# Kernel optimization log

Hardware: AMD Instinct MI355X
Metric: run time of the kernel (lower is better)

Reference implementation:

```python
import jax, jax.numpy as jnp
import numpy as np

N, D, H, DF = 2048, 1024, 16, 4096
DK = D // H
EPS = 1e-5


def layernorm(x, g, b):
    mu = jnp.mean(x, axis=-1, keepdims=True)
    var = jnp.mean((x - mu) ** 2, axis=-1, keepdims=True)
    return (x - mu) * jax.lax.rsqrt(var + EPS) * g + b


def setup_inputs() -> dict:
    key = jax.random.key(0)
    ks = jax.random.split(key, 8)
    s = 0.02
    return {
        "X": jax.random.normal(ks[0], (N, D), dtype=jnp.float32),
        "Wqkv": jax.random.normal(ks[1], (2 * D, D), dtype=jnp.float32) * s,
        "W1": jax.random.normal(ks[2], (DF, D), dtype=jnp.float32) * s,
        "b1": jnp.zeros((DF,), dtype=jnp.float32),
        "W2": jax.random.normal(ks[3], (D, DF), dtype=jnp.float32) * s,
        "b2": jnp.zeros((D,), dtype=jnp.float32),
        "g1": jnp.ones((D,), dtype=jnp.float32),
        "be1": jnp.zeros((D,), dtype=jnp.float32),
        "g2": jnp.ones((D,), dtype=jnp.float32),
        "be2": jnp.zeros((D,), dtype=jnp.float32),
    }


def reference(X, Wqkv, W1, b1, W2, b2, g1, be1, g2, be2):
    # shared-QK multi-head attention (Q == K), no bias
    qkv = X @ Wqkv.T                      # [N, 2D]
    qk, v = jnp.split(qkv, 2, axis=-1)    # [N, D] each
    qk = qk.reshape(N, H, DK)
    v = v.reshape(N, H, DK)
    scale = DK ** 0.5
    scores = jnp.einsum('nhd,mhd->hnm', qk, qk) / scale  # [H, N, N]
    att = jax.nn.softmax(scores, axis=-1)
    attn_out = jnp.einsum('hnm,mhd->nhd', att, v).reshape(N, D)
    # residual + LN, FFN (dropout is identity in eval), residual + LN
    h = layernorm(X + attn_out, g1, be1)
    ffn = jax.nn.relu(h @ W1.T + b1) @ W2.T + b2
    return layernorm(h + ffn, g2, be2)
```

## Files before the change

kernel.cpp:

```cpp
#include <hip/hip_runtime.h>
#include <stdint.h>


#define NTOK 2048
#define DMODEL 1024
#define NHEAD 16
#define DHEAD 64
#define DFF 4096

typedef __attribute__((ext_vector_type(8))) short short8;
typedef __attribute__((ext_vector_type(4))) short short4v;
typedef __attribute__((ext_vector_type(4))) float f32x4;

__device__ __forceinline__ float fexp2(float x) { return __builtin_amdgcn_exp2f(x); }

__device__ __forceinline__ short f2b(float f) {
  union { float f; unsigned u; } v; v.f = f;
  unsigned r = v.u + 0x7fffu + ((v.u >> 16) & 1u);
  return (short)(r >> 16);
}

__device__ __forceinline__ void gload_lds16(const void* g, void* l) {
  __builtin_amdgcn_global_load_lds((const __attribute__((address_space(1))) void*)g,
                                   (__attribute__((address_space(3))) void*)l,
                                   16, 0, 0);
}

__global__ void cast_all(const float* __restrict__ s0, short* __restrict__ d0, int n0,
                         const float* __restrict__ s1, short* __restrict__ d1, int n1,
                         const float* __restrict__ s2, short* __restrict__ d2, int n2,
                         const float* __restrict__ s3, short* __restrict__ d3, int n3) {
  int i = blockIdx.x * blockDim.x + threadIdx.x;
  const float* s; short* d; int j = i;
  if (j < n0) { s = s0; d = d0; }
  else { j -= n0;
    if (j < n1) { s = s1; d = d1; }
    else { j -= n1;
      if (j < n2) { s = s2; d = d2; }
      else { j -= n2; if (j >= n3) return; s = s3; d = d3; }
    }
  }
  const float4* p = (const float4*)(s + (size_t)j * 8);
  float4 a = p[0], b = p[1];
  short8 o;
  o[0] = f2b(a.x); o[1] = f2b(a.y); o[2] = f2b(a.z); o[3] = f2b(a.w);
  o[4] = f2b(b.x); o[5] = f2b(b.y); o[6] = f2b(b.z); o[7] = f2b(b.w);
  *(short8*)(d + (size_t)j * 8) = o;
}

template<int BM, int BN, int WR, int WC, bool BF16OUT, bool BIAS, bool RELU>
__launch_bounds__(WR * WC * 64, 2)
__global__ void gemm_bt(const short* __restrict__ A, const short* __restrict__ B,
                        const float* __restrict__ bias,
                        float* __restrict__ Cf, short* __restrict__ Cb,
                        int M, int N, int K, int lda, int ldb, int kstep) {
  constexpr int BK = 64;
  constexpr int THREADS = WR * WC * 64;
  constexpr int ACH = (BM * (BK / 8)) / THREADS;
  constexpr int BCH = (BN * (BK / 8)) / THREADS;
  constexpr int LPS = ACH + BCH;
  constexpr int MR = BM / (WR * 16);
  constexpr int NR = BN / (WC * 16);
  __shared__ short As[3][BM * BK];
  __shared__ short Bs[3][BN * BK];
  const int t = threadIdx.x;
  const int l = t & 63;
  const int w = t >> 6;
  const int wr = w / WC, wc = w % WC;
  const int lr = l & 15, lg = l >> 4;

  const int gx = gridDim.x, gy = gridDim.y;
  const int nxy = gx * gy;
  const int flat = blockIdx.x * gy + blockIdx.y;
  const int nf = (flat & 7) * (nxy >> 3) + (flat >> 3);
  const int bx = nf / gy, by = nf % gy;

  const int m0 = by * BM, n0 = bx * BN;
  const int koff = blockIdx.z * kstep;
  A += koff; B += koff;
  Cf += (size_t)blockIdx.z * M * N;

  auto stage = [&](int b, int k0) {
#pragma unroll
    for (int i = 0; i < ACH; ++i) {
      const int ci = i * THREADS + t;
      const int r = ci >> 3, c = ci & 7;
      const int cs = c ^ (r & 7);
      gload_lds16(A + (size_t)(m0 + r) * lda + k0 + cs * 8,
                  &As[b][(size_t)(i * THREADS + w * 64) * 8]);
    }
#pragma unroll
    for (int i = 0; i < BCH; ++i) {
      const int ci = i * THREADS + t;
      const int r = ci >> 3, c = ci & 7;
      const int cs = c ^ (r & 7);
      gload_lds16(B + (size_t)(n0 + r) * ldb + k0 + cs * 8,
                  &Bs[b][(size_t)(i * THREADS + w * 64) * 8]);
    }
  };

  f32x4 acc[MR][NR] = {};
  const int nIter = K / BK;
  stage(0, 0);
  if (1 < nIter) stage(1, BK);
  for (int it = 0; it < nIter; ++it) {
    const int cur = it % 3;
    if (it + 1 < nIter) {
      static_assert(LPS == 6, "vmcnt literal assumes 6 loads/stage");
      asm volatile("s_waitcnt vmcnt(6)" ::: "memory");
    } else {
      asm volatile("s_waitcnt vmcnt(0)" ::: "memory");
    }
    __builtin_amdgcn_sched_barrier(0);
    __builtin_amdgcn_s_barrier();
    __builtin_amdgcn_sched_barrier(0);
#pragma unroll
    for (int kk = 0; kk < 2; ++kk) {
      short8 a[MR], b[NR];
#pragma unroll
      for (int m = 0; m < MR; ++m) {
        const int r = wr * (BM / WR) + m * 16 + lr;
        a[m] = *(const short8*)(&As[cur][r * BK + (((kk * 4 + lg) ^ (r & 7)) * 8)]);
      }
#pragma unroll
      for (int n = 0; n < NR; ++n) {
        const int r = wc * (BN / WC) + n * 16 + lr;
        b[n] = *(const short8*)(&Bs[cur][r * BK + (((kk * 4 + lg) ^ (r & 7)) * 8)]);
      }
#pragma unroll
      for (int m = 0; m < MR; ++m)
#pragma unroll
        for (int n = 0; n < NR; ++n)
          acc[m][n] = __builtin_amdgcn_mfma_f32_16x16x32_bf16(a[m], b[n], acc[m][n], 0, 0, 0);
    }
    if (it + 2 < nIter) stage((it + 2) % 3, (it + 2) * BK);
  }
#pragma unroll
  for (int n = 0; n < NR; ++n) {
    const int col = n0 + wc * (BN / WC) + n * 16 + lr;
    const float bv = BIAS ? bias[col] : 0.0f;
#pragma unroll
    for (int m = 0; m < MR; ++m) {
#pragma unroll
      for (int r = 0; r < 4; ++r) {
        const int row = m0 + wr * (BM / WR) + m * 16 + lg * 4 + r;
        float v = acc[m][n][r] + bv;
        if (RELU) v = fmaxf(v, 0.0f);
        if (BF16OUT) Cb[(size_t)row * N + col] = f2b(v);
        else         Cf[(size_t)row * N + col] = v;
      }
    }
  }
}

__global__ void transpose_v(const short* __restrict__ src, short* __restrict__ dst) {
  __shared__ short tile[64][65];
  const int bx = blockIdx.x * 64;
  const int by = blockIdx.y * 64;
  const int t = threadIdx.x;
  const int tx = t & 63, ty = t >> 6;
#pragma unroll
  for (int i = 0; i < 64; i += 4)
    tile[ty + i][tx] = src[(size_t)(by + ty + i) * 2048 + 1024 + bx + tx];
  __syncthreads();
#pragma unroll
  for (int i = 0; i < 64; i += 4)
    dst[(size_t)(bx + ty + i) * 2048 + by + tx] = tile[tx][ty + i];
}

__launch_bounds__(256, 2)
__global__ void flash_attn(const short* __restrict__ qk, const short* __restrict__ vt,
                           float* __restrict__ O) {
  const int t = threadIdx.x;
  const int l = t & 63, w = t >> 6;
  const int lr = l & 15, lg = l >> 4;
  const int h = blockIdx.y;
  const int qb = blockIdx.x;
  __shared__ short Ks[2][64 * 64];
  __shared__ short Vs[2][64 * 64];
  __shared__ short Pl[4][16][72];
  const float C2 = 0.18033688011112042f;

  const int qrow = qb * 64 + w * 16 + lr;
  short8 aq[2];
#pragma unroll
  for (int f = 0; f < 2; ++f)
    aq[f] = *(const short8*)(qk + (size_t)qrow * 2048 + h * 64 + f * 32 + lg * 8);

  f32x4 o[4] = {};
  float mrun = -1e30f, lrun = 0.0f;

  auto stage = [&](int b, int kt) {
#pragma unroll
    for (int i = 0; i < 2; ++i) {
      const int chunk = i * 256 + w * 64 + l;
      const int r = chunk >> 3, c = chunk & 7;
      const int cs = c ^ (r & 7);
      gload_lds16(qk + (size_t)(kt * 64 + r) * 2048 + h * 64 + cs * 8,
                  &Ks[b][(size_t)(i * 256 + w * 64) * 8]);
    }
#pragma unroll
    for (int i = 0; i < 2; ++i) {
      const int chunk = i * 256 + w * 64 + l;
      const int r = chunk >> 3, c = chunk & 7;
      const int cs = c ^ (r & 7);
      gload_lds16(vt + (size_t)(h * 64 + r) * 2048 + kt * 64 + cs * 8,
                  &Vs[b][(size_t)(i * 256 + w * 64) * 8]);
    }
  };

  stage(0, 0);
  __syncthreads();

#pragma unroll 1
  for (int kt = 0; kt < 32; ++kt) {
    const int cur = kt & 1;
    if (kt + 1 < 32) stage(cur ^ 1, kt + 1);

    f32x4 s[4] = {};
    __builtin_amdgcn_s_setprio(1);
#pragma unroll
    for (int f = 0; f < 2; ++f) {
      short8 kf[4];
#pragma unroll
      for (int n = 0; n < 4; ++n) {
        const int r = n * 16 + lr;
        kf[n] = *(const short8*)(&Ks[cur][r * 64 + (((f * 4 + lg) ^ (lr & 7)) * 8)]);
      }
#pragma unroll
      for (int n = 0; n < 4; ++n)
        s[n] = __builtin_amdgcn_mfma_f32_16x16x32_bf16(kf[n], aq[f], s[n], 0, 0, 0);
    }
    __builtin_amdgcn_s_setprio(0);
    float m0 = fmaxf(fmaxf(s[0][0], s[0][1]), fmaxf(s[0][2], s[0][3]));
    float m1 = fmaxf(fmaxf(s[1][0], s[1][1]), fmaxf(s[1][2], s[1][3]));
    float m2 = fmaxf(fmaxf(s[2][0], s[2][1]), fmaxf(s[2][2], s[2][3]));
    float m3 = fmaxf(fmaxf(s[3][0], s[3][1]), fmaxf(s[3][2], s[3][3]));
    float tm = fmaxf(fmaxf(m0, m1), fmaxf(m2, m3));
    tm = fmaxf(tm, __shfl_xor(tm, 16));
    tm = fmaxf(tm, __shfl_xor(tm, 32));
    float corrv = 1.0f;
    if (__any(tm > mrun)) {
      const float mnew = fmaxf(mrun, tm);
      corrv = fexp2((mrun - mnew) * C2);
      mrun = mnew;
      f32x4 cov;
#pragma unroll
      for (int r = 0; r < 4; ++r)
        cov[r] = __shfl(corrv, lg * 4 + r);
#pragma unroll
      for (int n = 0; n < 4; ++n)
        o[n] *= cov;
    }
    float p[4][4];
#pragma unroll
    for (int n = 0; n < 4; ++n)
#pragma unroll
      for (int r = 0; r < 4; ++r)
        p[n][r] = fexp2((s[n][r] - mrun) * C2);
    float q0 = (p[0][0] + p[0][1]) + (p[0][2] + p[0][3]);
    float q1 = (p[1][0] + p[1][1]) + (p[1][2] + p[1][3]);
    float q2 = (p[2][0] + p[2][1]) + (p[2][2] + p[2][3]);
    float q3 = (p[3][0] + p[3][1]) + (p[3][2] + p[3][3]);
    float ps = (q0 + q1) + (q2 + q3);
    ps += __shfl_xor(ps, 16);
    ps += __shfl_xor(ps, 32);
    lrun = lrun * corrv + ps;
#pragma unroll
    for (int n = 0; n < 4; ++n) {
      uint2 wv;
      wv.x = ((unsigned)(unsigned short)f2b(p[n][1]) << 16) | (unsigned short)f2b(p[n][0]);
      wv.y = ((unsigned)(unsigned short)f2b(p[n][3]) << 16) | (unsigned short)f2b(p[n][2]);
      *(uint2*)&Pl[w][lr][n * 16 + lg * 4] = wv;
    }
    __builtin_amdgcn_s_setprio(1);
#pragma unroll
    for (int f = 0; f < 2; ++f) {
      short8 ap = *(const short8*)&Pl[w][lr][f * 32 + lg * 8];
      short8 vf[4];
#pragma unroll
      for (int n = 0; n < 4; ++n) {
        const int r = n * 16 + lr;
        vf[n] = *(const short8*)(&Vs[cur][r * 64 + (((f * 4 + lg) ^ (lr & 7)) * 8)]);
      }
#pragma unroll
      for (int n = 0; n < 4; ++n)
        o[n] = __builtin_amdgcn_mfma_f32_16x16x32_bf16(ap, vf[n], o[n], 0, 0, 0);
    }
    __builtin_amdgcn_s_setprio(0);
    __syncthreads();
  }

  f32x4 inv;
#pragma unroll
  for (int r = 0; r < 4; ++r)
    inv[r] = 1.0f / __shfl(lrun, lg * 4 + r);
#pragma unroll
  for (int n = 0; n < 4; ++n)
#pragma unroll
    for (int r = 0; r < 4; ++r)
      O[(size_t)(qb * 64 + w * 16 + lg * 4 + r) * 1024 + h * 64 + n * 16 + lr] = o[n][r] * inv[r];
}

__launch_bounds__(256)
__global__ void add_ln(const float* __restrict__ A, const float* __restrict__ B0,
                       const float* __restrict__ B1, const float* __restrict__ bias,
                       const float* __restrict__ g, const float* __restrict__ be,
                       float* __restrict__ outf, short* __restrict__ outb) {
  const int row = blockIdx.x;
  const int t = threadIdx.x;
  const size_t base = (size_t)row * 1024 + t * 4;
  float4 a = *(const float4*)(A + base);
  float4 b = *(const float4*)(B0 + base);
  float4 s; s.x = a.x + b.x; s.y = a.y + b.y; s.z = a.z + b.z; s.w = a.w + b.w;
  if (B1) {
    float4 c = *(const float4*)(B1 + base);
    s.x += c.x; s.y += c.y; s.z += c.z; s.w += c.w;
  }
  if (bias) {
    float4 c = *(const float4*)(bias + t * 4);
    s.x += c.x; s.y += c.y; s.z += c.z; s.w += c.w;
  }
  float sum = s.x + s.y + s.z + s.w;
  float sq  = s.x * s.x + s.y * s.y + s.z * s.z + s.w * s.w;
#pragma unroll
  for (int d = 32; d > 0; d >>= 1) {
    sum += __shfl_down(sum, d);
    sq  += __shfl_down(sq, d);
  }
  __shared__ float red[8];
  const int w = t >> 6, l = t & 63;
  if (l == 0) { red[w] = sum; red[4 + w] = sq; }
  __syncthreads();
  sum = red[0] + red[1] + red[2] + red[3];
  sq  = red[4] + red[5] + red[6] + red[7];
  const float mu = sum * (1.0f / 1024.0f);
  const float rstd = rsqrtf(sq * (1.0f / 1024.0f) - mu * mu + 1e-5f);
  float4 gv = *(const float4*)(g + t * 4);
  float4 bv = *(const float4*)(be + t * 4);
  float4 o;
  o.x = (s.x - mu) * rstd * gv.x + bv.x;
  o.y = (s.y - mu) * rstd * gv.y + bv.y;
  o.z = (s.z - mu) * rstd * gv.z + bv.z;
  o.w = (s.w - mu) * rstd * gv.w + bv.w;
  *(float4*)(outf + base) = o;
  if (outb) {
    short4v ob; ob.x = f2b(o.x); ob.y = f2b(o.y); ob.z = f2b(o.z); ob.w = f2b(o.w);
    *(short4v*)(outb + base) = ob;
  }
}

extern "C" void kernel_launch(void* const* d_in, const int* in_sizes, int n_in,
                              void* d_out, int out_size, void* d_ws, size_t ws_size,
                              hipStream_t stream) {
  const float* X    = (const float*)d_in[0];
  const float* Wqkv = (const float*)d_in[1];
  const float* W1   = (const float*)d_in[2];
  const float* b1   = (const float*)d_in[3];
  const float* W2   = (const float*)d_in[4];
  const float* b2   = (const float*)d_in[5];
  const float* g1   = (const float*)d_in[6];
  const float* be1  = (const float*)d_in[7];
  const float* g2   = (const float*)d_in[8];
  const float* be2  = (const float*)d_in[9];

  char* ws = (char*)d_ws;
  const size_t MiB = 1u << 20;
  short*  W1b   = (short*)(ws + 0 * MiB);
  short*  W2b   = (short*)(ws + 8 * MiB);
  float*  h     = (float*)(ws + 16 * MiB);
  short*  hb    = (short*)(ws + 24 * MiB);
  short*  qkvb  = (short*)(ws + 28 * MiB);
  short*  y1b   = (short*)(ws + 28 * MiB);
  short*  vt    = (short*)(ws + 36 * MiB);
  float*  attn  = (float*)(ws + 44 * MiB);
  float*  P0    = (float*)(ws + 44 * MiB);
  float*  P1    = P0 + (size_t)NTOK * DMODEL;
  short*  Xb    = (short*)(ws + 52 * MiB);
  short*  Wqkvb = (short*)(ws + 56 * MiB);

  cast_all<<<6144, 256, 0, stream>>>(X, Xb, NTOK * DMODEL / 8,
                                     Wqkv, Wqkvb, 2 * DMODEL * DMODEL / 8,
                                     W1, W1b, DFF * DMODEL / 8,
                                     W2, W2b, DMODEL * DFF / 8);

  {
    dim3 grid(2 * DMODEL / 128, NTOK / 64, 1);
    gemm_bt<64, 128, 2, 2, true, false, false><<<grid, 256, 0, stream>>>(
        Xb, Wqkvb, nullptr, nullptr, qkvb, NTOK, 2 * DMODEL, DMODEL, DMODEL, DMODEL, 0);
  }
  {
    dim3 grid(DMODEL / 64, NTOK / 64);
    transpose_v<<<grid, 256, 0, stream>>>(qkvb, vt);
  }
  {
    dim3 grid(NTOK / 64, NHEAD);
    flash_attn<<<grid, 256, 0, stream>>>(qkvb, vt, attn);
  }
  add_ln<<<NTOK, 256, 0, stream>>>(X, attn, nullptr, nullptr, g1, be1, h, hb);
  {
    dim3 grid(DFF / 128, NTOK / 64, 1);
    gemm_bt<64, 128, 2, 2, true, true, true><<<grid, 256, 0, stream>>>(
        hb, W1b, b1, nullptr, y1b, NTOK, DFF, DMODEL, DMODEL, DMODEL, 0);
  }
  {
    dim3 grid(DMODEL / 128, NTOK / 64, 2);
    gemm_bt<64, 128, 2, 2, false, false, false><<<grid, 256, 0, stream>>>(
        y1b, W2b, nullptr, P0, nullptr, NTOK, DMODEL, 2048, DFF, DFF, 2048);
  }
  add_ln<<<NTOK, 256, 0, stream>>>(h, P0, P1, b2, g2, be2, (float*)d_out, nullptr);
}
```

Before: 235.3 us.

## Process two query row groups per wave in flash attention to reuse K/V tiles

Each wave in the attention kernel now handles 32 query rows (two 16-row groups), so a block covers 128 queries and the grid halves. Each K and V fragment read from LDS feeds twice as many MFMAs, and global K/V staging per query drops by half. In exchange, register pressure roughly doubles for accumulators, and only 256 blocks are launched on a GPU with many CUs, which may reduce occupancy and parallelism.

Measured after the change: 247.4 us. +5.2%, slower.

```diff
diff --git a/kernel.cpp b/kernel.cpp
--- a/kernel.cpp
+++ b/kernel.cpp
@@ -178,17 +178,20 @@
   const int qb = blockIdx.x;
   __shared__ short Ks[2][64 * 64];
   __shared__ short Vs[2][64 * 64];
-  __shared__ short Pl[4][16][72];
+  __shared__ short Pl[4][2][16][72];
   const float C2 = 0.18033688011112042f;
 
-  const int qrow = qb * 64 + w * 16 + lr;
-  short8 aq[2];
-#pragma unroll
-  for (int f = 0; f < 2; ++f)
-    aq[f] = *(const short8*)(qk + (size_t)qrow * 2048 + h * 64 + f * 32 + lg * 8);
-
-  f32x4 o[4] = {};
-  float mrun = -1e30f, lrun = 0.0f;
+  short8 aq[2][2];
+#pragma unroll
+  for (int g = 0; g < 2; ++g) {
+    const int qrow = qb * 128 + w * 32 + g * 16 + lr;
+#pragma unroll
+    for (int f = 0; f < 2; ++f)
+      aq[g][f] = *(const short8*)(qk + (size_t)qrow * 2048 + h * 64 + f * 32 + lg * 8);
+  }
+
+  f32x4 o[2][4] = {};
+  float mrun[2] = {-1e30f, -1e30f}, lrun[2] = {0.0f, 0.0f};
 
   auto stage = [&](int b, int kt) {
 #pragma unroll
@@ -217,7 +220,7 @@
     const int cur = kt & 1;
     if (kt + 1 < 32) stage(cur ^ 1, kt + 1);
 
-    f32x4 s[4] = {};
+    f32x4 s[2][4] = {};
     __builtin_amdgcn_s_setprio(1);
 #pragma unroll
     for (int f = 0; f < 2; ++f) {
@@ -228,55 +231,63 @@
         kf[n] = *(const short8*)(&Ks[cur][r * 64 + (((f * 4 + lg) ^ (lr & 7)) * 8)]);
       }
 #pragma unroll
+      for (int g = 0; g < 2; ++g)
+#pragma unroll
+        for (int n = 0; n < 4; ++n)
+          s[g][n] = __builtin_amdgcn_mfma_f32_16x16x32_bf16(kf[n], aq[g][f], s[g][n], 0, 0, 0);
+    }
+    __builtin_amdgcn_s_setprio(0);
+
+#pragma unroll
+    for (int g = 0; g < 2; ++g) {
+      float m0 = fmaxf(fmaxf(s[g][0][0], s[g][0][1]), fmaxf(s[g][0][2], s[g][0][3]));
+      float m1 = fmaxf(fmaxf(s[g][1][0], s[g][1][1]), fmaxf(s[g][1][2], s[g][1][3]));
+      float m2 = fmaxf(fmaxf(s[g][2][0], s[g][2][1]), fmaxf(s[g][2][2], s[g][2][3]));
+      float m3 = fmaxf(fmaxf(s[g][3][0], s[g][3][1]), fmaxf(s[g][3][2], s[g][3][3]));
+      float tm = fmaxf(fmaxf(m0, m1), fmaxf(m2, m3));
+      tm = fmaxf(tm, __shfl_xor(tm, 16));
+      tm = fmaxf(tm, __shfl_xor(tm, 32));
+      float corrv = 1.0f;
+      if (__any(tm > mrun[g])) {
+        const float mnew = fmaxf(mrun[g], tm);
+        corrv = fexp2((mrun[g] - mnew) * C2);
+        mrun[g] = mnew;
+        f32x4 cov;
+#pragma unroll
+        for (int r = 0; r < 4; ++r)
+          cov[r] = __shfl(corrv, lg * 4 + r);
+#pragma unroll
+        for (int n = 0; n < 4; ++n)
+          o[g][n] *= cov;
+      }
+      float p[4][4];
+#pragma unroll
       for (int n = 0; n < 4; ++n)
-        s[n] = __builtin_amdgcn_mfma_f32_16x16x32_bf16(kf[n], aq[f], s[n], 0, 0, 0);
-    }
-    __builtin_amdgcn_s_setprio(0);
-    float m0 = fmaxf(fmaxf(s[0][0], s[0][1]), fmaxf(s[0][2], s[0][3]));
-    float m1 = fmaxf(fmaxf(s[1][0], s[1][1]), fmaxf(s[1][2], s[1][3]));
-    float m2 = fmaxf(fmaxf(s[2][0], s[2][1]), fmaxf(s[2][2], s[2][3]));
-    float m3 = fmaxf(fmaxf(s[3][0], s[3][1]), fmaxf(s[3][2], s[3][3]));
-    float tm = fmaxf(fmaxf(m0, m1), fmaxf(m2, m3));
-    tm = fmaxf(tm, __shfl_xor(tm, 16));
-    tm = fmaxf(tm, __shfl_xor(tm, 32));
-    float corrv = 1.0f;
-    if (__any(tm > mrun)) {
-      const float mnew = fmaxf(mrun, tm);
-      corrv = fexp2((mrun - mnew) * C2);
-      mrun = mnew;
-      f32x4 cov;
-#pragma unroll
-      for (int r = 0; r < 4; ++r)
-        cov[r] = __shfl(corrv, lg * 4 + r);
-#pragma unroll
-      for (int n = 0; n < 4; ++n)
-        o[n] *= cov;
-    }
-    float p[4][4];
-#pragma unroll
-    for (int n = 0; n < 4; ++n)
-#pragma unroll
-      for (int r = 0; r < 4; ++r)
-        p[n][r] = fexp2((s[n][r] - mrun) * C2);
-    float q0 = (p[0][0] + p[0][1]) + (p[0][2] + p[0][3]);
-    float q1 = (p[1][0] + p[1][1]) + (p[1][2] + p[1][3]);
-    float q2 = (p[2][0] + p[2][1]) + (p[2][2] + p[2][3]);
-    float q3 = (p[3][0] + p[3][1]) + (p[3][2] + p[3][3]);
-    float ps = (q0 + q1) + (q2 + q3);
-    ps += __shfl_xor(ps, 16);
-    ps += __shfl_xor(ps, 32);
-    lrun = lrun * corrv + ps;
-#pragma unroll
-    for (int n = 0; n < 4; ++n) {
-      uint2 wv;
-      wv.x = ((unsigned)(unsigned short)f2b(p[n][1]) << 16) | (unsigned short)f2b(p[n][0]);
-      wv.y = ((unsigned)(unsigned short)f2b(p[n][3]) << 16) | (unsigned short)f2b(p[n][2]);
-      *(uint2*)&Pl[w][lr][n * 16 + lg * 4] = wv;
-    }
+#pragma unroll
+        for (int r = 0; r < 4; ++r)
+          p[n][r] = fexp2((s[g][n][r] - mrun[g]) * C2);
+      float q0 = (p[0][0] + p[0][1]) + (p[0][2] + p[0][3]);
+      float q1 = (p[1][0] + p[1][1]) + (p[1][2] + p[1][3]);
+      float q2 = (p[2][0] + p[2][1]) + (p[2][2] + p[2][3]);
+      float q3 = (p[3][0] + p[3][1]) + (p[3][2] + p[3][3]);
+      float ps = (q0 + q1) + (q2 + q3);
+      ps += __shfl_xor(ps, 16);
+      ps += __shfl_xor(ps, 32);
+      lrun[g] = lrun[g] * corrv + ps;
+#pragma unroll
+      for (int n = 0; n < 4; ++n) {
+        uint2 wv;
+        wv.x = ((unsigned)(unsigned short)f2b(p[n][1]) << 16) | (unsigned short)f2b(p[n][0]);
+        wv.y = ((unsigned)(unsigned short)f2b(p[n][3]) << 16) | (unsigned short)f2b(p[n][2]);
+        *(uint2*)&Pl[w][g][lr][n * 16 + lg * 4] = wv;
+      }
+    }
+
     __builtin_amdgcn_s_setprio(1);
 #pragma unroll
     for (int f = 0; f < 2; ++f) {
-      short8 ap = *(const short8*)&Pl[w][lr][f * 32 + lg * 8];
+      short8 ap0 = *(const short8*)&Pl[w][0][lr][f * 32 + lg * 8];
+      short8 ap1 = *(const short8*)&Pl[w][1][lr][f * 32 + lg * 8];
       short8 vf[4];
 #pragma unroll
       for (int n = 0; n < 4; ++n) {
@@ -284,22 +295,28 @@
         vf[n] = *(const short8*)(&Vs[cur][r * 64 + (((f * 4 + lg) ^ (lr & 7)) * 8)]);
       }
 #pragma unroll
-      for (int n = 0; n < 4; ++n)
-        o[n] = __builtin_amdgcn_mfma_f32_16x16x32_bf16(ap, vf[n], o[n], 0, 0, 0);
+      for (int n = 0; n < 4; ++n) {
+        o[0][n] = __builtin_amdgcn_mfma_f32_16x16x32_bf16(ap0, vf[n], o[0][n], 0, 0, 0);
+        o[1][n] = __builtin_amdgcn_mfma_f32_16x16x32_bf16(ap1, vf[n], o[1][n], 0, 0, 0);
+      }
     }
     __builtin_amdgcn_s_setprio(0);
     __syncthreads();
   }
 
-  f32x4 inv;
-#pragma unroll
-  for (int r = 0; r < 4; ++r)
-    inv[r] = 1.0f / __shfl(lrun, lg * 4 + r);
-#pragma unroll
-  for (int n = 0; n < 4; ++n)
+#pragma unroll
+  for (int g = 0; g < 2; ++g) {
+    f32x4 inv;
 #pragma unroll
     for (int r = 0; r < 4; ++r)
-      O[(size_t)(qb * 64 + w * 16 + lg * 4 + r) * 1024 + h * 64 + n * 16 + lr] = o[n][r] * inv[r];
+      inv[r] = 1.0f / __shfl(lrun[g], lg * 4 + r);
+#pragma unroll
+    for (int n = 0; n < 4; ++n)
+#pragma unroll
+      for (int r = 0; r < 4; ++r)
+        O[(size_t)(qb * 128 + w * 32 + g * 16 + lg * 4 + r) * 1024 + h * 64 + n * 16 + lr] =
+            o[g][n][r] * inv[r];
+  }
 }
 
 __launch_bounds__(256)
@@ -394,7 +411,7 @@
     transpose_v<<<grid, 256, 0, stream>>>(qkvb, vt);
   }
   {
-    dim3 grid(NTOK / 64, NHEAD);
+    dim3 grid(NTOK / 128, NHEAD);
     flash_attn<<<grid, 256, 0, stream>>>(qkvb, vt, attn);
   }
   add_ln<<<NTOK, 256, 0, stream>>>(X, attn, nullptr, nullptr, g1, be1, h, hb);
```
